# Optimization experiments

Hardware: AMD Instinct MI355X
Metric: run time of the kernel (lower is better)

Reference implementation:

```python
import jax, jax.numpy as jnp
import numpy as np

DIM, HEADS = 1024, 16
B, N = 2, 2048


def setup_inputs() -> dict:
    key = jax.random.key(0)
    ks = jax.random.split(key, 8)
    d = DIM // HEADS
    return {
        "x": jax.random.normal(ks[0], (B, N, DIM), dtype=jnp.float32),
        "w_qkv": jax.random.normal(ks[1], (DIM, 3 * DIM), dtype=jnp.float32) * (DIM ** -0.5),
        "w_out": jax.random.normal(ks[2], (DIM, DIM), dtype=jnp.float32) * (DIM ** -0.5),
        "b_out": jnp.zeros((DIM,), dtype=jnp.float32),
        "void_q": jax.random.normal(ks[3], (1, HEADS, 1, d), dtype=jnp.float32),
        "void_k": jax.random.normal(ks[4], (1, HEADS, 1, d), dtype=jnp.float32),
        "void_v": jax.random.normal(ks[5], (1, HEADS, 1, d), dtype=jnp.float32),
        "attention_trace": jax.random.uniform(ks[6], (HEADS, 1, 1), dtype=jnp.float32),
        "temperature_factor": jax.random.normal(ks[7], (HEADS, 1, 1), dtype=jnp.float32),
    }


def reference(x, w_qkv, w_out, b_out, void_q, void_k, void_v,
              attention_trace, temperature_factor):
    b, n, dim = x.shape
    h = void_q.shape[1]
    d = dim // h

    qkv = x @ w_qkv  # [b, n, 3*dim]
    q, k, v = jnp.split(qkv, 3, axis=-1)

    def to_heads(t):
        return t.reshape(b, n, h, d).transpose(0, 2, 1, 3)  # b h n d

    q, k, v = to_heads(q), to_heads(k), to_heads(v)

    # append the void token to q, k, v -> seq length n+1
    q = jnp.concatenate([q, jnp.broadcast_to(void_q, (b, h, 1, d))], axis=2)
    k = jnp.concatenate([k, jnp.broadcast_to(void_k, (b, h, 1, d))], axis=2)
    v = jnp.concatenate([v, jnp.broadcast_to(void_v, (b, h, 1, d))], axis=2)

    # NOTE: original scales by full dim**-0.5, not head-dim
    dots = jnp.einsum('bhid,bhjd->bhij', q, k) * (dim ** -0.5)
    # void-to-void bias of +10 at index [n, n]
    dots = dots.at[:, :, n, n].add(10.0)

    # stateful per-head temperature (trace is a buffer, treated as input)
    temperature = jnp.maximum(1.0 + jnp.abs(attention_trace) * temperature_factor, 1.0)  # [h,1,1]
    attn = jax.nn.softmax(dots / temperature, axis=-1)  # [b, h, n+1, n+1]

    out = jnp.einsum('bhij,bhjd->bhid', attn, v)[:, :, :n, :]  # drop void row
    out = out.transpose(0, 2, 1, 3).reshape(b, n, dim)  # b n (h d)
    return out @ w_out + b_out
```

## Files before the change

kernel.cpp:

```cpp
#include <hip/hip_runtime.h>
#include <stdint.h>

#define DIMF   1024
#define HEADS  16
#define HD     64
#define BB     2
#define NN     2048
#define NKP    2112
#define NTILE  33

typedef __attribute__((ext_vector_type(8))) __bf16 bf16x8;
typedef __attribute__((ext_vector_type(4))) float  f32x4;

__device__ __forceinline__ float b2f(uint16_t h) {
  union { uint32_t u; float f; } v; v.u = ((uint32_t)h) << 16; return v.f;
}
__device__ __forceinline__ uint16_t f2b(float f) {
  union { float f; uint32_t u; } v; v.f = f;
  uint32_t r = v.u + 0x7FFFu + ((v.u >> 16) & 1u);
  return (uint16_t)(r >> 16);
}

__device__ __forceinline__ void gl_lds16(const void* g, void* l) {
  __builtin_amdgcn_global_load_lds(
      (const __attribute__((address_space(1))) void*)g,
      (__attribute__((address_space(3))) void*)l, 16, 0, 0);
}

__global__ __launch_bounds__(256) void prep_k(const float* __restrict__ x,
                                              uint16_t* __restrict__ x_bf,
                                              const float* __restrict__ vk,
                                              const float* __restrict__ vv,
                                              uint16_t* __restrict__ k_ws,
                                              uint16_t* __restrict__ vt_ws,
                                              const float* __restrict__ wqkv,
                                              uint16_t* __restrict__ wqkvT,
                                              const float* __restrict__ wout,
                                              uint16_t* __restrict__ woutT) {
  __shared__ uint16_t tile[32][33];
  const int blk = blockIdx.x;
  if (blk < 4096) {
    int i = blk * 256 + threadIdx.x;
    float4 v = *(const float4*)&x[(size_t)i * 4];
    uint16_t* d = x_bf + (size_t)i * 4;
    d[0] = f2b(v.x); d[1] = f2b(v.y); d[2] = f2b(v.z); d[3] = f2b(v.w);
  } else if (blk < 4608) {
    int idx = (blk - 4096) * 256 + threadIdx.x;
    int dd = idx & 63;
    int r  = (idx >> 6) & 63;
    int bh = idx >> 12;
    int h  = bh & (HEADS - 1);
    uint16_t kv  = (r == 0) ? f2b(vk[h * HD + dd]) : (uint16_t)0;
    uint16_t vvv = (r == 0) ? f2b(vv[h * HD + dd]) : (uint16_t)0;
    k_ws[((size_t)bh * NKP + NN + r) * HD + dd]  = kv;
    vt_ws[((size_t)bh * HD + dd) * NKP + NN + r] = vvv;
  } else {
    int tb = blk - 4608;
    const float* src; uint16_t* dst; int N, bx, by;
    if (tb < 3072) { src = wqkv; dst = wqkvT; N = 3072; bx = (tb % 96) * 32; by = (tb / 96) * 32; }
    else { tb -= 3072; src = wout; dst = woutT; N = 1024; bx = (tb % 32) * 32; by = (tb / 32) * 32; }
    const int M = 1024;
    int xx = threadIdx.x & 31, y0 = (threadIdx.x >> 5) * 4;
#pragma unroll
    for (int i = 0; i < 4; ++i)
      tile[y0 + i][xx] = f2b(src[(size_t)(by + y0 + i) * N + bx + xx]);
    __syncthreads();
#pragma unroll
    for (int i = 0; i < 4; ++i)
      dst[(size_t)(bx + y0 + i) * M + by + xx] = tile[xx][y0 + i];
  }
}

__global__ __launch_bounds__(256) void gemm0_k(const uint16_t* __restrict__ A,
                                               const uint16_t* __restrict__ Bt,
                                               int K,
                                               uint16_t* __restrict__ o0,
                                               uint16_t* __restrict__ o1,
                                               uint16_t* __restrict__ o2) {
  __shared__ uint16_t lds_a[128][64];
  __shared__ uint16_t lds_b[128][64];
  const int m0 = blockIdx.y * 128, n0 = blockIdx.x * 128;
  const int tid = threadIdx.x, lane = tid & 63, wid = tid >> 6;
  const int wm = (wid >> 1) * 64, wn = (wid & 1) * 64;
  const int lr = lane & 15, lg = lane >> 4;

  const int rsw = (lr & 7) << 4;
  const int rc0 = (lg * 16) ^ rsw;
  const int rc1 = (64 + lg * 16) ^ rsw;

  f32x4 acc[4][4] = {};
  for (int k0 = 0; k0 < K; k0 += 64) {
    __syncthreads();
#pragma unroll
    for (int it = 0; it < 4; ++it) {
      const int chunk = wid * 4 + it;
      const int o = chunk * 1024 + lane * 16;
      const int r = o >> 7, cb = o & 127;
      const int scb = cb ^ ((r & 7) << 4);
      gl_lds16((const char*)&A[(size_t)(m0 + r) * K + k0] + scb,
               (char*)&lds_a[0][0] + chunk * 1024);
      gl_lds16((const char*)&Bt[(size_t)(n0 + r) * K + k0] + scb,
               (char*)&lds_b[0][0] + chunk * 1024);
    }
    __syncthreads();
    bf16x8 af[4][2], bf[4][2];
#pragma unroll
    for (int i = 0; i < 4; ++i) {
      const char* ra = (const char*)&lds_a[0][0] + (wm + i * 16 + lr) * 128;
      af[i][0] = *(const bf16x8*)(ra + rc0);
      af[i][1] = *(const bf16x8*)(ra + rc1);
    }
#pragma unroll
    for (int j = 0; j < 4; ++j) {
      const char* rb = (const char*)&lds_b[0][0] + (wn + j * 16 + lr) * 128;
      bf[j][0] = *(const bf16x8*)(rb + rc0);
      bf[j][1] = *(const bf16x8*)(rb + rc1);
    }
#pragma unroll
    for (int kk = 0; kk < 2; ++kk)
#pragma unroll
      for (int i = 0; i < 4; ++i)
#pragma unroll
        for (int j = 0; j < 4; ++j)
          acc[i][j] = __builtin_amdgcn_mfma_f32_16x16x32_bf16(af[i][kk], bf[j][kk],
                                                              acc[i][j], 0, 0, 0);
  }
#pragma unroll
  for (int i = 0; i < 4; ++i)
#pragma unroll
    for (int j = 0; j < 4; ++j)
#pragma unroll
      for (int r = 0; r < 4; ++r) {
        int mg = m0 + wm + i * 16 + lg * 4 + r;
        int ng = n0 + wn + j * 16 + lr;
        int b = mg >> 11, n = mg & (NN - 1);
        int which = ng >> 10, rem = ng & (DIMF - 1), h = rem >> 6, dd = rem & 63;
        int bh = b * HEADS + h;
        uint16_t bv = f2b(acc[i][j][r]);
        if (which == 0)      o0[((size_t)bh * NN + n) * HD + dd] = bv;
        else if (which == 1) o1[((size_t)bh * NKP + n) * HD + dd] = bv;
        else                 o2[((size_t)bh * HD + dd) * NKP + n] = bv;
      }
}

__global__ __launch_bounds__(256) void gemm1_k(const uint16_t* __restrict__ A,
                                               const uint16_t* __restrict__ Bt,
                                               int K,
                                               float* __restrict__ fo,
                                               const float* __restrict__ bias) {
  __shared__ uint16_t lds_a[64][64];
  __shared__ uint16_t lds_b[128][64];
  const int m0 = blockIdx.y * 64, n0 = blockIdx.x * 128;
  const int tid = threadIdx.x, lane = tid & 63, wid = tid >> 6;
  const int wm = (wid >> 1) * 32, wn = (wid & 1) * 64;
  const int lr = lane & 15, lg = lane >> 4;

  const int rsw = (lr & 7) << 4;
  const int rc0 = (lg * 16) ^ rsw;
  const int rc1 = (64 + lg * 16) ^ rsw;

  f32x4 acc[2][4] = {};
  for (int k0 = 0; k0 < K; k0 += 64) {
    __syncthreads();
#pragma unroll
    for (int it = 0; it < 6; ++it) {
      const int c = wid * 6 + it;
      const int o = (c & 7) * 1024 + lane * 16;
      if (c < 8) {
        const int r = o >> 7, cb = o & 127;
        const int scb = cb ^ ((r & 7) << 4);
        gl_lds16((const char*)&A[(size_t)(m0 + r) * K + k0] + scb,
                 (char*)&lds_a[0][0] + c * 1024);
      } else {
        const int o2 = (c - 8) * 1024 + lane * 16;
        const int r = o2 >> 7, cb = o2 & 127;
        const int scb = cb ^ ((r & 7) << 4);
        gl_lds16((const char*)&Bt[(size_t)(n0 + r) * K + k0] + scb,
                 (char*)&lds_b[0][0] + (c - 8) * 1024);
      }
    }
    __syncthreads();
    bf16x8 af[2][2], bf[4][2];
#pragma unroll
    for (int i = 0; i < 2; ++i) {
      const char* ra = (const char*)&lds_a[0][0] + (wm + i * 16 + lr) * 128;
      af[i][0] = *(const bf16x8*)(ra + rc0);
      af[i][1] = *(const bf16x8*)(ra + rc1);
    }
#pragma unroll
    for (int j = 0; j < 4; ++j) {
      const char* rb = (const char*)&lds_b[0][0] + (wn + j * 16 + lr) * 128;
      bf[j][0] = *(const bf16x8*)(rb + rc0);
      bf[j][1] = *(const bf16x8*)(rb + rc1);
    }
#pragma unroll
    for (int kk = 0; kk < 2; ++kk)
#pragma unroll
      for (int i = 0; i < 2; ++i)
#pragma unroll
        for (int j = 0; j < 4; ++j)
          acc[i][j] = __builtin_amdgcn_mfma_f32_16x16x32_bf16(af[i][kk], bf[j][kk],
                                                              acc[i][j], 0, 0, 0);
  }
#pragma unroll
  for (int i = 0; i < 2; ++i)
#pragma unroll
    for (int j = 0; j < 4; ++j)
#pragma unroll
      for (int r = 0; r < 4; ++r) {
        int mg = m0 + wm + i * 16 + lg * 4 + r;
        int ng = n0 + wn + j * 16 + lr;
        fo[(size_t)mg * DIMF + ng] = acc[i][j][r] + bias[ng];
      }
}

__global__ __launch_bounds__(512) void attn_k(const uint16_t* __restrict__ q_ws,
                                              const uint16_t* __restrict__ k_ws,
                                              const uint16_t* __restrict__ vt_ws,
                                              const float* __restrict__ trace,
                                              const float* __restrict__ factor,
                                              uint16_t* __restrict__ o_ws) {
  __shared__ uint16_t ldsk[64][64];
  __shared__ uint16_t ldsv[64][64];
  __shared__ uint16_t ldsp[8][16][72];
  const int bh = blockIdx.x;
  const int qb = blockIdx.y;
  const int h = bh & (HEADS - 1), b = bh >> 4;
  const int tid = threadIdx.x, lane = tid & 63, wid = tid >> 6;
  const int lr = lane & 15, lg = lane >> 4;

  const float temp  = fmaxf(1.0f + fabsf(trace[h]) * factor[h], 1.0f);
  const float scale = 0.03125f / temp;

  const int qrow0 = qb * 128 + wid * 16;
  const uint16_t* qrow = q_ws + ((size_t)bh * NN + qrow0 + lr) * HD;
  bf16x8 qf[2];
  qf[0] = *(const bf16x8*)(qrow + lg * 8);
  qf[1] = *(const bf16x8*)(qrow + 32 + lg * 8);

  const int rsw = (lr & 7) << 4;
  const char* kb0 = (const char*)&ldsk[0][0] + lr * 128 + ((lg * 16) ^ rsw);
  const char* kb1 = (const char*)&ldsk[0][0] + lr * 128 + ((64 + lg * 16) ^ rsw);
  const char* vb0 = (const char*)&ldsv[0][0] + lr * 128 + ((lg * 16) ^ rsw);
  const char* vb1 = (const char*)&ldsv[0][0] + lr * 128 + ((64 + lg * 16) ^ rsw);
  const char* pr  = (const char*)&ldsp[wid][lr][lg * 8];

  f32x4 acc[4] = {};
  float lsum[4] = {0.f, 0.f, 0.f, 0.f};

  for (int t = 0; t < NTILE; ++t) {
    const int t0 = t * 64;
    __syncthreads();
    {
      const int chunk = wid;
      const int o = chunk * 1024 + lane * 16;
      const int r = o >> 7, cb = o & 127;
      const int scb = cb ^ ((r & 7) << 4);
      gl_lds16((const char*)&k_ws[((size_t)bh * NKP + t0 + r) * HD] + scb,
               (char*)&ldsk[0][0] + chunk * 1024);
      gl_lds16((const char*)&vt_ws[((size_t)bh * HD + r) * NKP + t0] + scb,
               (char*)&ldsv[0][0] + chunk * 1024);
    }
    __syncthreads();

    f32x4 s[4];
#pragma unroll
    for (int c = 0; c < 4; ++c) {
      bf16x8 kf0 = *(const bf16x8*)(kb0 + c * 2048);
      bf16x8 kf1 = *(const bf16x8*)(kb1 + c * 2048);
      f32x4 sa = {};
      __builtin_amdgcn_s_setprio(1);
      sa = __builtin_amdgcn_mfma_f32_16x16x32_bf16(qf[0], kf0, sa, 0, 0, 0);
      sa = __builtin_amdgcn_mfma_f32_16x16x32_bf16(qf[1], kf1, sa, 0, 0, 0);
      __builtin_amdgcn_s_setprio(0);
      s[c] = sa;
    }
#pragma unroll
    for (int c = 0; c < 4; ++c)
#pragma unroll
      for (int r = 0; r < 4; ++r) {
        union { float f; uint32_t u; } pv;
        pv.f = __expf(s[c][r] * scale);
        ldsp[wid][lg * 4 + r][c * 16 + lr] = (uint16_t)(pv.u >> 16);
        pv.u &= 0xffff0000u;
        lsum[r] += pv.f;
      }
    asm volatile("" ::: "memory");
    __builtin_amdgcn_sched_barrier(0);
    __builtin_amdgcn_s_setprio(1);
#pragma unroll
    for (int kk = 0; kk < 2; ++kk) {
      bf16x8 pf = *(const bf16x8*)(pr + kk * 64);
#pragma unroll
      for (int cd = 0; cd < 4; ++cd) {
        bf16x8 vf = *(const bf16x8*)((kk ? vb1 : vb0) + cd * 2048);
        acc[cd] = __builtin_amdgcn_mfma_f32_16x16x32_bf16(pf, vf, acc[cd], 0, 0, 0);
      }
    }
    __builtin_amdgcn_s_setprio(0);
  }
#pragma unroll
  for (int r = 0; r < 4; ++r) {
    float l = lsum[r];
    l += __shfl_xor(l, 1); l += __shfl_xor(l, 2);
    l += __shfl_xor(l, 4); l += __shfl_xor(l, 8);
    l -= 63.0f;
    const float inv = 1.0f / l;
    const int n = qrow0 + lg * 4 + r;
    size_t base = ((size_t)b * NN + n) * DIMF + h * HD;
#pragma unroll
    for (int cd = 0; cd < 4; ++cd)
      o_ws[base + cd * 16 + lr] = f2b(acc[cd][r] * inv);
  }
}

extern "C" void kernel_launch(void* const* d_in, const int* in_sizes, int n_in,
                              void* d_out, int out_size, void* d_ws, size_t ws_size,
                              hipStream_t stream) {
  const float* x      = (const float*)d_in[0];
  const float* wqkv   = (const float*)d_in[1];
  const float* wout   = (const float*)d_in[2];
  const float* bout   = (const float*)d_in[3];
  const float* voidk  = (const float*)d_in[5];
  const float* voidv  = (const float*)d_in[6];
  const float* trace  = (const float*)d_in[7];
  const float* factor = (const float*)d_in[8];
  float* out = (float*)d_out;

  uint16_t* ws    = (uint16_t*)d_ws;
  uint16_t* x_bf  = ws;
  uint16_t* o_ws  = x_bf;
  uint16_t* wqkvT = x_bf  + 4194304;
  uint16_t* woutT = wqkvT + 3145728;
  uint16_t* q_ws  = woutT + 1048576;
  uint16_t* k_ws  = q_ws  + 4194304;
  uint16_t* vt_ws = k_ws  + 4325376;

  prep_k<<<dim3(8704), dim3(256), 0, stream>>>(x, x_bf, voidk, voidv, k_ws, vt_ws,
                                               wqkv, wqkvT, wout, woutT);
  gemm0_k<<<dim3(3072 / 128, 4096 / 128), dim3(256), 0, stream>>>(
      x_bf, wqkvT, 1024, q_ws, k_ws, vt_ws);
  attn_k<<<dim3(HEADS * BB, NN / 128), dim3(512), 0, stream>>>(
      q_ws, k_ws, vt_ws, trace, factor, o_ws);
  gemm1_k<<<dim3(1024 / 128, 4096 / 64), dim3(256), 0, stream>>>(
      o_ws, woutT, 1024, out, bout);
}
```

Before: 129.2 us.

## Use 128-key attention tiles and fold softmax scale into Q projection

Doubles the attention key/value tile from 64 to 128 keys, which halves the tile count and the barriers per tile. The padding grows to 127 phantom zero keys, and their contribution is subtracted from the row sum. The softmax scale, temperature and log2(e) factor are folded into the Q output of the QKV GEMM, so attention uses exp2 directly and skips a multiply per score. Scores are now exponentiated right after each MFMA chunk rather than after all chunks. The costs are more padded work (127 versus 63 phantom keys), larger LDS use per block, and extra precision loss from scaling Q before the bf16 rounding.

```diff
diff --git a/kernel.cpp b/kernel.cpp
--- a/kernel.cpp
+++ b/kernel.cpp
@@ -6,8 +6,9 @@
 #define HD     64
 #define BB     2
 #define NN     2048
-#define NKP    2112
-#define NTILE  33
+#define NKP    2176
+#define NTILE  17
+#define NPHANT 127.0f
 
 typedef __attribute__((ext_vector_type(8))) __bf16 bf16x8;
 typedef __attribute__((ext_vector_type(4))) float  f32x4;
@@ -44,18 +45,18 @@
     float4 v = *(const float4*)&x[(size_t)i * 4];
     uint16_t* d = x_bf + (size_t)i * 4;
     d[0] = f2b(v.x); d[1] = f2b(v.y); d[2] = f2b(v.z); d[3] = f2b(v.w);
-  } else if (blk < 4608) {
+  } else if (blk < 5120) {
     int idx = (blk - 4096) * 256 + threadIdx.x;
     int dd = idx & 63;
-    int r  = (idx >> 6) & 63;
-    int bh = idx >> 12;
+    int r  = (idx >> 6) & 127;
+    int bh = idx >> 13;
     int h  = bh & (HEADS - 1);
     uint16_t kv  = (r == 0) ? f2b(vk[h * HD + dd]) : (uint16_t)0;
     uint16_t vvv = (r == 0) ? f2b(vv[h * HD + dd]) : (uint16_t)0;
     k_ws[((size_t)bh * NKP + NN + r) * HD + dd]  = kv;
     vt_ws[((size_t)bh * HD + dd) * NKP + NN + r] = vvv;
   } else {
-    int tb = blk - 4608;
+    int tb = blk - 5120;
     const float* src; uint16_t* dst; int N, bx, by;
     if (tb < 3072) { src = wqkv; dst = wqkvT; N = 3072; bx = (tb % 96) * 32; by = (tb / 96) * 32; }
     else { tb -= 3072; src = wout; dst = woutT; N = 1024; bx = (tb % 32) * 32; by = (tb / 32) * 32; }
@@ -76,7 +77,9 @@
                                                int K,
                                                uint16_t* __restrict__ o0,
                                                uint16_t* __restrict__ o1,
-                                               uint16_t* __restrict__ o2) {
+                                               uint16_t* __restrict__ o2,
+                                               const float* __restrict__ trace,
+                                               const float* __restrict__ factor) {
   __shared__ uint16_t lds_a[128][64];
   __shared__ uint16_t lds_b[128][64];
   const int m0 = blockIdx.y * 128, n0 = blockIdx.x * 128;
@@ -136,7 +139,12 @@
         int b = mg >> 11, n = mg & (NN - 1);
         int which = ng >> 10, rem = ng & (DIMF - 1), h = rem >> 6, dd = rem & 63;
         int bh = b * HEADS + h;
-        uint16_t bv = f2b(acc[i][j][r]);
+        float v = acc[i][j][r];
+        if (which == 0) {
+          float tmp = fmaxf(1.0f + fabsf(trace[h]) * factor[h], 1.0f);
+          v *= 0.04508422f / tmp;
+        }
+        uint16_t bv = f2b(v);
         if (which == 0)      o0[((size_t)bh * NN + n) * HD + dd] = bv;
         else if (which == 1) o1[((size_t)bh * NKP + n) * HD + dd] = bv;
         else                 o2[((size_t)bh * HD + dd) * NKP + n] = bv;
@@ -165,8 +173,8 @@
 #pragma unroll
     for (int it = 0; it < 6; ++it) {
       const int c = wid * 6 + it;
-      const int o = (c & 7) * 1024 + lane * 16;
       if (c < 8) {
+        const int o = c * 1024 + lane * 16;
         const int r = o >> 7, cb = o & 127;
         const int scb = cb ^ ((r & 7) << 4);
         gl_lds16((const char*)&A[(size_t)(m0 + r) * K + k0] + scb,
@@ -217,21 +225,16 @@
 __global__ __launch_bounds__(512) void attn_k(const uint16_t* __restrict__ q_ws,
                                               const uint16_t* __restrict__ k_ws,
                                               const uint16_t* __restrict__ vt_ws,
-                                              const float* __restrict__ trace,
-                                              const float* __restrict__ factor,
                                               uint16_t* __restrict__ o_ws) {
-  __shared__ uint16_t ldsk[64][64];
-  __shared__ uint16_t ldsv[64][64];
-  __shared__ uint16_t ldsp[8][16][72];
+  __shared__ uint16_t ldsk[128][64];
+  __shared__ uint16_t ldsv[64][128];
+  __shared__ uint16_t ldsp[8][16][136];
   const int bh = blockIdx.x;
   const int qb = blockIdx.y;
   const int h = bh & (HEADS - 1), b = bh >> 4;
   const int tid = threadIdx.x, lane = tid & 63, wid = tid >> 6;
   const int lr = lane & 15, lg = lane >> 4;
 
-  const float temp  = fmaxf(1.0f + fabsf(trace[h]) * factor[h], 1.0f);
-  const float scale = 0.03125f / temp;
-
   const int qrow0 = qb * 128 + wid * 16;
   const uint16_t* qrow = q_ws + ((size_t)bh * NN + qrow0 + lr) * HD;
   bf16x8 qf[2];
@@ -241,31 +244,35 @@
   const int rsw = (lr & 7) << 4;
   const char* kb0 = (const char*)&ldsk[0][0] + lr * 128 + ((lg * 16) ^ rsw);
   const char* kb1 = (const char*)&ldsk[0][0] + lr * 128 + ((64 + lg * 16) ^ rsw);
-  const char* vb0 = (const char*)&ldsv[0][0] + lr * 128 + ((lg * 16) ^ rsw);
-  const char* vb1 = (const char*)&ldsv[0][0] + lr * 128 + ((64 + lg * 16) ^ rsw);
-  const char* pr  = (const char*)&ldsp[wid][lr][lg * 8];
+  const char* vbs = (const char*)&ldsv[0][0] + lr * 256;
+  int voff[4];
+#pragma unroll
+  for (int kk = 0; kk < 4; ++kk) voff[kk] = (kk * 64 + lg * 16) ^ rsw;
+  const char* pr = (const char*)&ldsp[wid][lr][lg * 8];
 
   f32x4 acc[4] = {};
   float lsum[4] = {0.f, 0.f, 0.f, 0.f};
 
   for (int t = 0; t < NTILE; ++t) {
-    const int t0 = t * 64;
-    __syncthreads();
-    {
-      const int chunk = wid;
+    const int t0 = t * 128;
+    __syncthreads();
+#pragma unroll
+    for (int it = 0; it < 2; ++it) {
+      const int chunk = wid * 2 + it;
       const int o = chunk * 1024 + lane * 16;
-      const int r = o >> 7, cb = o & 127;
-      const int scb = cb ^ ((r & 7) << 4);
-      gl_lds16((const char*)&k_ws[((size_t)bh * NKP + t0 + r) * HD] + scb,
-               (char*)&ldsk[0][0] + chunk * 1024);
-      gl_lds16((const char*)&vt_ws[((size_t)bh * HD + r) * NKP + t0] + scb,
-               (char*)&ldsv[0][0] + chunk * 1024);
-    }
-    __syncthreads();
-
-    f32x4 s[4];
-#pragma unroll
-    for (int c = 0; c < 4; ++c) {
+      { const int r = o >> 7, cb = o & 127;
+        const int scb = cb ^ ((r & 7) << 4);
+        gl_lds16((const char*)&k_ws[((size_t)bh * NKP + t0 + r) * HD] + scb,
+                 (char*)&ldsk[0][0] + chunk * 1024); }
+      { const int r = o >> 8, cb = o & 255;
+        const int scb = cb ^ ((r & 7) << 4);
+        gl_lds16((const char*)&vt_ws[((size_t)bh * HD + r) * NKP + t0] + scb,
+                 (char*)&ldsv[0][0] + chunk * 1024); }
+    }
+    __syncthreads();
+
+#pragma unroll
+    for (int c = 0; c < 8; ++c) {
       bf16x8 kf0 = *(const bf16x8*)(kb0 + c * 2048);
       bf16x8 kf1 = *(const bf16x8*)(kb1 + c * 2048);
       f32x4 sa = {};
@@ -273,27 +280,24 @@
       sa = __builtin_amdgcn_mfma_f32_16x16x32_bf16(qf[0], kf0, sa, 0, 0, 0);
       sa = __builtin_amdgcn_mfma_f32_16x16x32_bf16(qf[1], kf1, sa, 0, 0, 0);
       __builtin_amdgcn_s_setprio(0);
-      s[c] = sa;
-    }
-#pragma unroll
-    for (int c = 0; c < 4; ++c)
 #pragma unroll
       for (int r = 0; r < 4; ++r) {
         union { float f; uint32_t u; } pv;
-        pv.f = __expf(s[c][r] * scale);
+        pv.f = exp2f(sa[r]);
         ldsp[wid][lg * 4 + r][c * 16 + lr] = (uint16_t)(pv.u >> 16);
         pv.u &= 0xffff0000u;
         lsum[r] += pv.f;
       }
+    }
     asm volatile("" ::: "memory");
     __builtin_amdgcn_sched_barrier(0);
     __builtin_amdgcn_s_setprio(1);
 #pragma unroll
-    for (int kk = 0; kk < 2; ++kk) {
+    for (int kk = 0; kk < 4; ++kk) {
       bf16x8 pf = *(const bf16x8*)(pr + kk * 64);
 #pragma unroll
       for (int cd = 0; cd < 4; ++cd) {
-        bf16x8 vf = *(const bf16x8*)((kk ? vb1 : vb0) + cd * 2048);
+        bf16x8 vf = *(const bf16x8*)(vbs + cd * 4096 + voff[kk]);
         acc[cd] = __builtin_amdgcn_mfma_f32_16x16x32_bf16(pf, vf, acc[cd], 0, 0, 0);
       }
     }
@@ -304,7 +308,7 @@
     float l = lsum[r];
     l += __shfl_xor(l, 1); l += __shfl_xor(l, 2);
     l += __shfl_xor(l, 4); l += __shfl_xor(l, 8);
-    l -= 63.0f;
+    l -= NPHANT;
     const float inv = 1.0f / l;
     const int n = qrow0 + lg * 4 + r;
     size_t base = ((size_t)b * NN + n) * DIMF + h * HD;
@@ -334,14 +338,14 @@
   uint16_t* woutT = wqkvT + 3145728;
   uint16_t* q_ws  = woutT + 1048576;
   uint16_t* k_ws  = q_ws  + 4194304;
-  uint16_t* vt_ws = k_ws  + 4325376;
-
-  prep_k<<<dim3(8704), dim3(256), 0, stream>>>(x, x_bf, voidk, voidv, k_ws, vt_ws,
+  uint16_t* vt_ws = k_ws  + 4456448;
+
+  prep_k<<<dim3(9216), dim3(256), 0, stream>>>(x, x_bf, voidk, voidv, k_ws, vt_ws,
                                                wqkv, wqkvT, wout, woutT);
   gemm0_k<<<dim3(3072 / 128, 4096 / 128), dim3(256), 0, stream>>>(
-      x_bf, wqkvT, 1024, q_ws, k_ws, vt_ws);
+      x_bf, wqkvT, 1024, q_ws, k_ws, vt_ws, trace, factor);
   attn_k<<<dim3(HEADS * BB, NN / 128), dim3(512), 0, stream>>>(
-      q_ws, k_ws, vt_ws, trace, factor, o_ws);
+      q_ws, k_ws, vt_ws, o_ws);
   gemm1_k<<<dim3(1024 / 128, 4096 / 64), dim3(256), 0, stream>>>(
       o_ws, woutT, 1024, out, bout);
 }
```

Result: slower. 163.6 us (+26.7%).
